# Performance work log

Measured on AMD Instinct MI355X. Metric: run time of the kernel, lower is better.

Reference implementation:

```python
import jax, jax.numpy as jnp
import numpy as np

N_NODES = 50000


def _add_self_loops(edge_index, n):
    loop = jnp.arange(n, dtype=edge_index.dtype)
    src = jnp.concatenate([edge_index[0], loop])
    dst = jnp.concatenate([edge_index[1], loop])
    return src, dst


def _gcn_norm(src, dst, n):
    # symmetric normalization with unit edge weights (edge_weight=None)
    w = jnp.ones(src.shape[0], dtype=jnp.float32)
    deg = jax.ops.segment_sum(w, dst, num_segments=n)  # [N]
    dinv = jnp.where(deg > 0, jax.lax.rsqrt(jnp.maximum(deg, 1.0)), 0.0)
    return dinv[src] * w * dinv[dst]  # [E+N]


def _gcn_conv(x, src, dst, norm, W, b, n):
    h = x @ W                                   # [N, out] transform first (PyG order)
    msg = h[src] * norm[:, None]                # [E+N, out] gather + scale
    agg = jax.ops.segment_sum(msg, dst, num_segments=n)  # scatter-add
    return agg + b


def setup_inputs() -> dict:
    key = jax.random.key(0)
    k1, k2, k3, k4 = jax.random.split(key, 4)
    N, E, IN, HID, OUT = N_NODES, 1600000, 512, 64, 7
    x = jax.random.normal(k1, (N, IN), dtype=jnp.float32)
    edge_index = jax.random.randint(k2, (2, E), 0, N, dtype=jnp.int64)
    W1 = jax.random.normal(k3, (IN, HID), dtype=jnp.float32) * (1.0 / np.sqrt(IN))
    b1 = jnp.zeros((HID,), dtype=jnp.float32)
    W2 = jax.random.normal(k4, (HID, OUT), dtype=jnp.float32) * (1.0 / np.sqrt(HID))
    b2 = jnp.zeros((OUT,), dtype=jnp.float32)
    return {"x": x, "edge_index": edge_index, "W1": W1, "b1": b1, "W2": W2, "b2": b2}


def reference(x, edge_index, W1, b1, W2, b2):
    n = x.shape[0]
    src, dst = _add_self_loops(edge_index, n)
    norm = _gcn_norm(src, dst, n)  # graph-only, shared across layers
    h = _gcn_conv(x, src, dst, norm, W1, b1, n)
    h = jax.nn.relu(h)
    # dropout is identity in eval/inference mode
    out = _gcn_conv(h, src, dst, norm, W2, b2, n)
    return out
```

## Files before the change

### kernel.cpp

```cpp
#include <hip/hip_runtime.h>

#define N_NODES 50000
#define N_EDGES 1600000
#define DIM_IN  512
#define DIM_HID 64
#define DIM_OUT 7
#define NBUCK   196
#define PART_BLOCKS 256

using u16 = unsigned short;
using bf16x8 = __attribute__((ext_vector_type(8))) __bf16;
using f32x4  = __attribute__((ext_vector_type(4))) float;

__device__ __forceinline__ float bf2f(u16 u) {
    union { float f; unsigned int i; } v;
    v.i = ((unsigned int)u) << 16;
    return v.f;
}

__device__ __forceinline__ u16 f2bf(float f) {
    union { float f; unsigned int i; } v;
    v.f = f;
    unsigned int r = 0x7FFFu + ((v.i >> 16) & 1u);
    return (u16)((v.i + r) >> 16);
}

__global__ void k_detect(const u16* __restrict__ xw, const int* __restrict__ ei32,
                         int* __restrict__ flags) {
    if (threadIdx.x == 0 && blockIdx.x == 0) {
        int sane = 0;
        for (int i = 0; i < 256; ++i) {
            u16 w = xw[2 * i];
            int e = (w >> 7) & 0xFF;
            if (e >= 100 && e <= 140) sane++;
        }
        flags[0] = (sane >= 200) ? 0 : 1;
        int nz = 0;
        for (int i = 0; i < 256; ++i)
            if (ei32[2 * i + 1] != 0) nz++;
        flags[1] = (nz == 0) ? 1 : 0;
    }
}

__device__ __forceinline__ int ld_edge(const int* ei, int i64f, size_t idx) {
    if (i64f) return (int)((const long long*)ei)[idx];
    return ei[idx];
}

__global__ void k_count(const int* __restrict__ ei, const int* __restrict__ flags,
                        int* __restrict__ gbsum, int* __restrict__ cnt) {
    __shared__ int hist[NBUCK];
    int t = threadIdx.x;
    int i64f = flags[1];
    const int CH = (N_EDGES + PART_BLOCKS - 1) / PART_BLOCKS;
    int lo = blockIdx.x * CH;
    int hi = lo + CH; if (hi > N_EDGES) hi = N_EDGES;
    if (t < NBUCK) hist[t] = 0;
    __syncthreads();
    for (int i = lo + t; i < hi; i += 256) {
        int s = ld_edge(ei, i64f, (size_t)i);
        int d = ld_edge(ei, i64f, (size_t)N_EDGES + i);
        if ((unsigned)d < (unsigned)N_NODES && (unsigned)s < (unsigned)N_NODES)
            atomicAdd(&hist[d >> 8], 1);
    }
    __syncthreads();
    if (t < NBUCK) {
        int h = hist[t];
        cnt[t * PART_BLOCKS + blockIdx.x] = h;
        if (h > 0) atomicAdd(&gbsum[t], h);
    }
}

__global__ void k_s2(const int* __restrict__ gbsum, int* __restrict__ bbase,
                     int* __restrict__ rowptr) {
    __shared__ int sc[256];
    int t = threadIdx.x;
    int v = (t < NBUCK) ? gbsum[t] : 0;
    sc[t] = v;
    __syncthreads();
    for (int off = 1; off < 256; off <<= 1) {
        int u = (t >= off) ? sc[t - off] : 0;
        __syncthreads();
        sc[t] += u;
        __syncthreads();
    }
    if (t < NBUCK) bbase[t] = sc[t] - v;
    if (t == 255) rowptr[N_NODES] = sc[255];
}

__global__ void k_pb(const int* __restrict__ bbase, int* __restrict__ cnt) {
    __shared__ int sc[256];
    int b = blockIdx.x, t = threadIdx.x;
    int v = cnt[b * PART_BLOCKS + t];
    sc[t] = v;
    __syncthreads();
    for (int off = 1; off < 256; off <<= 1) {
        int u = (t >= off) ? sc[t - off] : 0;
        __syncthreads();
        sc[t] += u;
        __syncthreads();
    }
    cnt[b * PART_BLOCKS + t] = bbase[b] + sc[t] - v;
}

__global__ void k_part(const int* __restrict__ ei, const int* __restrict__ flags,
                       const int* __restrict__ cnt, unsigned int* __restrict__ ebuf) {
    __shared__ int cur[NBUCK];
    int t = threadIdx.x, blk = blockIdx.x;
    int i64f = flags[1];
    const int CH = (N_EDGES + PART_BLOCKS - 1) / PART_BLOCKS;
    int lo = blk * CH;
    int hi = lo + CH; if (hi > N_EDGES) hi = N_EDGES;
    if (t < NBUCK) cur[t] = cnt[t * PART_BLOCKS + blk];
    __syncthreads();
    for (int i = lo + t; i < hi; i += 256) {
        int s = ld_edge(ei, i64f, (size_t)i);
        int d = ld_edge(ei, i64f, (size_t)N_EDGES + i);
        if ((unsigned)d < (unsigned)N_NODES && (unsigned)s < (unsigned)N_NODES) {
            int pos = atomicAdd(&cur[d >> 8], 1);
            if ((unsigned)pos < (unsigned)N_EDGES)
                ebuf[pos] = ((unsigned)s << 8) | (unsigned)(d & 255);
        }
    }
}

__global__ void k_cfill(const unsigned int* __restrict__ ebuf,
                        const int* __restrict__ bbase, const int* __restrict__ gbsum,
                        int* __restrict__ rowptr, float* __restrict__ dinv,
                        int* __restrict__ col) {
    __shared__ int dcnt[256];
    __shared__ int sc[256];
    __shared__ int cur[256];
    int b = blockIdx.x, t = threadIdx.x;
    int e0 = bbase[b];
    int e1 = e0 + gbsum[b];
    dcnt[t] = 0;
    __syncthreads();
    for (int e = e0 + t; e < e1; e += 256)
        atomicAdd(&dcnt[ebuf[e] & 255u], 1);
    __syncthreads();
    int v = dcnt[t];
    sc[t] = v;
    __syncthreads();
    for (int off = 1; off < 256; off <<= 1) {
        int u = (t >= off) ? sc[t - off] : 0;
        __syncthreads();
        sc[t] += u;
        __syncthreads();
    }
    int row0 = e0 + sc[t] - v;
    cur[t] = row0;
    int idx = b * 256 + t;
    if (idx < N_NODES) {
        rowptr[idx] = row0;
        dinv[idx] = rsqrtf((float)(v + 1));
    }
    __syncthreads();
    for (int e = e0 + t; e < e1; e += 256) {
        unsigned int x = ebuf[e];
        int p = atomicAdd(&cur[x & 255u], 1);
        if ((unsigned)p < (unsigned)N_EDGES) col[p] = (int)(x >> 8);
    }
}

__global__ void k_tw1(const void* __restrict__ W1, const int* __restrict__ flags,
                      u16* __restrict__ W1T) {
    int i = blockIdx.x * blockDim.x + threadIdx.x;
    if (i < DIM_IN * DIM_HID) {
        int n = i >> 9;
        int k = i & 511;
        if (flags[0]) W1T[i] = f2bf(((const float*)W1)[k * DIM_HID + n]);
        else          W1T[i] = ((const u16*)W1)[k * DIM_HID + n];
    }
}

__launch_bounds__(256)
__global__ void k_gemm1(const void* __restrict__ xraw, const u16* __restrict__ W1T,
                        const int* __restrict__ flags, const float* __restrict__ dinv,
                        u16* __restrict__ hs) {
    int f32f = flags[0];
    int wave = threadIdx.x >> 6;
    int lane = threadIdx.x & 63;
    int m16 = lane & 15;
    int quad = lane >> 4;
    int rbase = blockIdx.x * 64 + wave * 16;
    int ra = rbase + m16;
    if (ra > N_NODES - 1) ra = N_NODES - 1;
    const u16*   xrow_b = (const u16*)xraw   + (size_t)ra * DIM_IN + quad * 8;
    const float* xrow_f = (const float*)xraw + (size_t)ra * DIM_IN + quad * 8;
    const u16* wrow = W1T + (size_t)m16 * DIM_IN + quad * 8;

    f32x4 acc0 = {0.f, 0.f, 0.f, 0.f};
    f32x4 acc1 = {0.f, 0.f, 0.f, 0.f};
    f32x4 acc2 = {0.f, 0.f, 0.f, 0.f};
    f32x4 acc3 = {0.f, 0.f, 0.f, 0.f};

    for (int ks = 0; ks < DIM_IN / 32; ++ks) {
        bf16x8 a;
        if (f32f) {
            const float4* q = reinterpret_cast<const float4*>(xrow_f + ks * 32);
            float4 p0 = q[0], p1 = q[1];
            union { bf16x8 v; u16 s[8]; } u;
            u.s[0] = f2bf(p0.x); u.s[1] = f2bf(p0.y); u.s[2] = f2bf(p0.z); u.s[3] = f2bf(p0.w);
            u.s[4] = f2bf(p1.x); u.s[5] = f2bf(p1.y); u.s[6] = f2bf(p1.z); u.s[7] = f2bf(p1.w);
            a = u.v;
        } else {
            a = *reinterpret_cast<const bf16x8*>(xrow_b + ks * 32);
        }
        bf16x8 b0 = *reinterpret_cast<const bf16x8*>(wrow + ks * 32);
        bf16x8 b1 = *reinterpret_cast<const bf16x8*>(wrow + ks * 32 + 16 * DIM_IN);
        bf16x8 b2 = *reinterpret_cast<const bf16x8*>(wrow + ks * 32 + 32 * DIM_IN);
        bf16x8 b3 = *reinterpret_cast<const bf16x8*>(wrow + ks * 32 + 48 * DIM_IN);
        acc0 = __builtin_amdgcn_mfma_f32_16x16x32_bf16(a, b0, acc0, 0, 0, 0);
        acc1 = __builtin_amdgcn_mfma_f32_16x16x32_bf16(a, b1, acc1, 0, 0, 0);
        acc2 = __builtin_amdgcn_mfma_f32_16x16x32_bf16(a, b2, acc2, 0, 0, 0);
        acc3 = __builtin_amdgcn_mfma_f32_16x16x32_bf16(a, b3, acc3, 0, 0, 0);
    }

#pragma unroll
    for (int i = 0; i < 4; ++i) {
        int r = rbase + quad * 4 + i;
        if (r < N_NODES) {
            float dv = dinv[r];
            u16* orow = hs + (size_t)r * DIM_HID;
            orow[ 0 + m16] = f2bf(acc0[i] * dv);
            orow[16 + m16] = f2bf(acc1[i] * dv);
            orow[32 + m16] = f2bf(acc2[i] * dv);
            orow[48 + m16] = f2bf(acc3[i] * dv);
        }
    }
}

__launch_bounds__(256)
__global__ void k_agg1(const u16* __restrict__ hs, const int* __restrict__ rowptr,
                       const int* __restrict__ col, const float* __restrict__ dinv,
                       const void* __restrict__ b1, const void* __restrict__ W2,
                       const int* __restrict__ flags, float* __restrict__ zs) {
    int f32f = flags[0];
    int wave = threadIdx.x >> 6;
    int lane = threadIdx.x & 63;
    int d = blockIdx.x * 4 + wave;
    if (d >= N_NODES) return;
    int start = rowptr[d], end = rowptr[d + 1];
    if (start < 0) start = 0;
    if (end > N_EDGES) end = N_EDGES;
    if (end < start) end = start;

    float acc = 0.f;
    int n8 = (end - start) >> 3;
    int cA[8];
    if (n8 > 0) {
        const int* cp = col + start;
#pragma unroll
        for (int j = 0; j < 8; ++j) cA[j] = cp[j];
        for (int it = 0; it < n8; ++it) {
            int cB[8];
            if (it + 1 < n8) {
                const int* cpn = col + start + (it + 1) * 8;
#pragma unroll
                for (int j = 0; j < 8; ++j) cB[j] = cpn[j];
            } else {
#pragma unroll
                for (int j = 0; j < 8; ++j) cB[j] = 0;
            }
            float v[8];
#pragma unroll
            for (int j = 0; j < 8; ++j) v[j] = bf2f(hs[(size_t)cA[j] * DIM_HID + lane]);
#pragma unroll
            for (int j = 0; j < 8; ++j) acc += v[j];
#pragma unroll
            for (int j = 0; j < 8; ++j) cA[j] = cB[j];
        }
    }
    for (int e = start + n8 * 8; e < end; ++e)
        acc += bf2f(hs[(size_t)col[e] * DIM_HID + lane]);
    acc += bf2f(hs[(size_t)d * DIM_HID + lane]);

    float b1v = f32f ? ((const float*)b1)[lane] : bf2f(((const u16*)b1)[lane]);
    float dv = dinv[d];
    float h2 = fmaxf(acc * dv + b1v, 0.f);

    float p[7];
#pragma unroll
    for (int f = 0; f < 7; ++f) {
        float w = f32f ? ((const float*)W2)[lane * DIM_OUT + f]
                       : bf2f(((const u16*)W2)[lane * DIM_OUT + f]);
        p[f] = h2 * w;
    }
#pragma unroll
    for (int off = 32; off >= 1; off >>= 1) {
#pragma unroll
        for (int f = 0; f < 7; ++f) p[f] += __shfl_xor(p[f], off);
    }
    if (lane == 0) {
#pragma unroll
        for (int f = 0; f < 7; ++f) zs[(size_t)d * 8 + f] = p[f] * dv;
        zs[(size_t)d * 8 + 7] = 0.f;
    }
}

__launch_bounds__(256)
__global__ void k_agg2(const float* __restrict__ zs, const int* __restrict__ rowptr,
                       const int* __restrict__ col, const float* __restrict__ dinv,
                       const void* __restrict__ b2, const int* __restrict__ flags,
                       float* __restrict__ out) {
    int f32f = flags[0];
    int wave = threadIdx.x >> 6;
    int lane = threadIdx.x & 63;
    int d = blockIdx.x * 4 + wave;
    if (d >= N_NODES) return;
    int f = lane & 7;
    int g = lane >> 3;
    int start = rowptr[d], end = rowptr[d + 1];
    if (start < 0) start = 0;
    if (end > N_EDGES) end = N_EDGES;
    if (end < start) end = start;

    float acc = 0.f;
    for (int e = start + g; e < end; e += 8)
        acc += zs[(size_t)col[e] * 8 + f];

    acc += __shfl_xor(acc, 8);
    acc += __shfl_xor(acc, 16);
    acc += __shfl_xor(acc, 32);

    if (lane < 7) {
        float b2v = f32f ? ((const float*)b2)[lane] : bf2f(((const u16*)b2)[lane]);
        float tot = (acc + zs[(size_t)d * 8 + lane]) * dinv[d] + b2v;
        out[(size_t)d * DIM_OUT + lane] = tot;
    }
}

extern "C" void kernel_launch(void* const* d_in, const int* in_sizes, int n_in,
                              void* d_out, int out_size, void* d_ws, size_t ws_size,
                              hipStream_t stream) {
    const void* x  = d_in[0];
    const int*  ei = (const int*)d_in[1];
    const void* W1 = d_in[2];
    const void* b1 = d_in[3];
    const void* W2 = d_in[4];
    const void* b2 = d_in[5];

    char* ws = (char*)d_ws;
    size_t off = 0;
    auto alloc = [&](size_t bytes) -> void* {
        void* p = ws + off;
        off = (off + bytes + 255) & ~(size_t)255;
        return p;
    };
    int*   flags  = (int*)alloc(32);
    int*   rowptr = (int*)alloc((size_t)(N_NODES + 1) * 4);
    int*   gbsum  = (int*)alloc((size_t)NBUCK * 4);
    int*   bbase  = (int*)alloc((size_t)NBUCK * 4);
    int*   cnt    = (int*)alloc((size_t)NBUCK * PART_BLOCKS * 4);
    float* dinv   = (float*)alloc((size_t)N_NODES * 4);
    u16*   W1T    = (u16*)alloc((size_t)DIM_IN * DIM_HID * 2);
    unsigned int* ebuf = (unsigned int*)alloc((size_t)N_EDGES * 4);
    int*   colb   = (int*)alloc((size_t)N_EDGES * 4);
    u16*   hs     = (u16*)alloc((size_t)N_NODES * DIM_HID * 2);
    float* zs     = (float*)alloc((size_t)N_NODES * 8 * 4);
    float* out    = (float*)d_out;

    hipMemsetAsync(gbsum, 0, (size_t)NBUCK * 4, stream);
    k_detect<<<1, 64, 0, stream>>>((const u16*)x, ei, flags);
    k_count<<<PART_BLOCKS, 256, 0, stream>>>(ei, flags, gbsum, cnt);
    k_s2   <<<1, 256, 0, stream>>>(gbsum, bbase, rowptr);
    k_pb   <<<NBUCK, 256, 0, stream>>>(bbase, cnt);
    k_part <<<PART_BLOCKS, 256, 0, stream>>>(ei, flags, cnt, ebuf);
    k_cfill<<<NBUCK, 256, 0, stream>>>(ebuf, bbase, gbsum, rowptr, dinv, colb);
    k_tw1  <<<(DIM_IN * DIM_HID + 255) / 256, 256, 0, stream>>>(W1, flags, W1T);
    k_gemm1<<<(N_NODES + 63) / 64, 256, 0, stream>>>(x, W1T, flags, dinv, hs);
    k_agg1 <<<(N_NODES + 3) / 4, 256, 0, stream>>>(hs, rowptr, colb, dinv, b1, W2, flags, zs);
    k_agg2 <<<(N_NODES + 3) / 4, 256, 0, stream>>>(zs, rowptr, colb, dinv, b2, flags, out);
}
```

Measured before the change: 347.1 us.

## Parallelize detect, merge scan kernels, widen CSR blocks, shuffle-broadcast agg1 indices

Several changes land together. The flag detection becomes a parallel shared-memory reduction, and the separate bucket-scan kernel is folded into k_pb, which now recomputes the global scan in every block. The CSR-build kernels (count, part, cfill) launch 1024-thread blocks instead of 256, and int64 edge loads read only the low 32-bit word. In k_agg1 each lane loads one column index per 64 edges and broadcasts it with shuffles, gathering 16 rows per step to raise memory-level parallelism. The costs are extra cross-lane shuffles and a redundant per-block scan, and the int64 load now assumes little-endian indices that fit in 32 bits.

```diff
diff --git a/kernel.cpp b/kernel.cpp
--- a/kernel.cpp
+++ b/kernel.cpp
@@ -27,23 +27,26 @@
 
 __global__ void k_detect(const u16* __restrict__ xw, const int* __restrict__ ei32,
                          int* __restrict__ flags) {
-    if (threadIdx.x == 0 && blockIdx.x == 0) {
-        int sane = 0;
-        for (int i = 0; i < 256; ++i) {
-            u16 w = xw[2 * i];
-            int e = (w >> 7) & 0xFF;
-            if (e >= 100 && e <= 140) sane++;
-        }
-        flags[0] = (sane >= 200) ? 0 : 1;
-        int nz = 0;
-        for (int i = 0; i < 256; ++i)
-            if (ei32[2 * i + 1] != 0) nz++;
-        flags[1] = (nz == 0) ? 1 : 0;
+    __shared__ int s1[256];
+    __shared__ int s2[256];
+    int t = threadIdx.x;
+    u16 w = xw[2 * t];
+    int e = (w >> 7) & 0xFF;
+    s1[t] = (e >= 100 && e <= 140) ? 1 : 0;
+    s2[t] = (ei32[2 * t + 1] != 0) ? 1 : 0;
+    __syncthreads();
+    for (int off = 128; off >= 1; off >>= 1) {
+        if (t < off) { s1[t] += s1[t + off]; s2[t] += s2[t + off]; }
+        __syncthreads();
+    }
+    if (t == 0) {
+        flags[0] = (s1[0] >= 200) ? 0 : 1;
+        flags[1] = (s2[0] == 0) ? 1 : 0;
     }
 }
 
 __device__ __forceinline__ int ld_edge(const int* ei, int i64f, size_t idx) {
-    if (i64f) return (int)((const long long*)ei)[idx];
+    if (i64f) return ei[2 * idx];
     return ei[idx];
 }
 
@@ -57,7 +60,7 @@
     int hi = lo + CH; if (hi > N_EDGES) hi = N_EDGES;
     if (t < NBUCK) hist[t] = 0;
     __syncthreads();
-    for (int i = lo + t; i < hi; i += 256) {
+    for (int i = lo + t; i < hi; i += 1024) {
         int s = ld_edge(ei, i64f, (size_t)i);
         int d = ld_edge(ei, i64f, (size_t)N_EDGES + i);
         if ((unsigned)d < (unsigned)N_NODES && (unsigned)s < (unsigned)N_NODES)
@@ -71,11 +74,26 @@
     }
 }
 
-__global__ void k_s2(const int* __restrict__ gbsum, int* __restrict__ bbase,
-                     int* __restrict__ rowptr) {
+__global__ void k_pb(const int* __restrict__ gbsum, int* __restrict__ cnt,
+                     int* __restrict__ bbase, int* __restrict__ rowptr) {
+    __shared__ int g0[256];
+    __shared__ int gs[256];
     __shared__ int sc[256];
-    int t = threadIdx.x;
-    int v = (t < NBUCK) ? gbsum[t] : 0;
+    int b = blockIdx.x, t = threadIdx.x;
+    int gv = (t < NBUCK) ? gbsum[t] : 0;
+    g0[t] = gv;
+    gs[t] = gv;
+    __syncthreads();
+    for (int off = 1; off < 256; off <<= 1) {
+        int u = (t >= off) ? gs[t - off] : 0;
+        __syncthreads();
+        gs[t] += u;
+        __syncthreads();
+    }
+    int bb = gs[b] - g0[b];
+    if (t == 0) bbase[b] = bb;
+    if (b == 0 && t == 255) rowptr[N_NODES] = gs[255];
+    int v = cnt[b * PART_BLOCKS + t];
     sc[t] = v;
     __syncthreads();
     for (int off = 1; off < 256; off <<= 1) {
@@ -84,23 +102,7 @@
         sc[t] += u;
         __syncthreads();
     }
-    if (t < NBUCK) bbase[t] = sc[t] - v;
-    if (t == 255) rowptr[N_NODES] = sc[255];
-}
-
-__global__ void k_pb(const int* __restrict__ bbase, int* __restrict__ cnt) {
-    __shared__ int sc[256];
-    int b = blockIdx.x, t = threadIdx.x;
-    int v = cnt[b * PART_BLOCKS + t];
-    sc[t] = v;
-    __syncthreads();
-    for (int off = 1; off < 256; off <<= 1) {
-        int u = (t >= off) ? sc[t - off] : 0;
-        __syncthreads();
-        sc[t] += u;
-        __syncthreads();
-    }
-    cnt[b * PART_BLOCKS + t] = bbase[b] + sc[t] - v;
+    cnt[b * PART_BLOCKS + t] = bb + sc[t] - v;
 }
 
 __global__ void k_part(const int* __restrict__ ei, const int* __restrict__ flags,
@@ -113,7 +115,7 @@
     int hi = lo + CH; if (hi > N_EDGES) hi = N_EDGES;
     if (t < NBUCK) cur[t] = cnt[t * PART_BLOCKS + blk];
     __syncthreads();
-    for (int i = lo + t; i < hi; i += 256) {
+    for (int i = lo + t; i < hi; i += 1024) {
         int s = ld_edge(ei, i64f, (size_t)i);
         int d = ld_edge(ei, i64f, (size_t)N_EDGES + i);
         if ((unsigned)d < (unsigned)N_NODES && (unsigned)s < (unsigned)N_NODES) {
@@ -134,29 +136,31 @@
     int b = blockIdx.x, t = threadIdx.x;
     int e0 = bbase[b];
     int e1 = e0 + gbsum[b];
-    dcnt[t] = 0;
-    __syncthreads();
-    for (int e = e0 + t; e < e1; e += 256)
+    if (t < 256) dcnt[t] = 0;
+    __syncthreads();
+    for (int e = e0 + t; e < e1; e += 1024)
         atomicAdd(&dcnt[ebuf[e] & 255u], 1);
     __syncthreads();
-    int v = dcnt[t];
-    sc[t] = v;
+    int v = 0;
+    if (t < 256) { v = dcnt[t]; sc[t] = v; }
     __syncthreads();
     for (int off = 1; off < 256; off <<= 1) {
-        int u = (t >= off) ? sc[t - off] : 0;
-        __syncthreads();
-        sc[t] += u;
-        __syncthreads();
-    }
-    int row0 = e0 + sc[t] - v;
-    cur[t] = row0;
-    int idx = b * 256 + t;
-    if (idx < N_NODES) {
-        rowptr[idx] = row0;
-        dinv[idx] = rsqrtf((float)(v + 1));
-    }
-    __syncthreads();
-    for (int e = e0 + t; e < e1; e += 256) {
+        int u = (t >= off && t < 256) ? sc[t - off] : 0;
+        __syncthreads();
+        if (t < 256) sc[t] += u;
+        __syncthreads();
+    }
+    if (t < 256) {
+        int row0 = e0 + sc[t] - v;
+        cur[t] = row0;
+        int idx = b * 256 + t;
+        if (idx < N_NODES) {
+            rowptr[idx] = row0;
+            dinv[idx] = rsqrtf((float)(v + 1));
+        }
+    }
+    __syncthreads();
+    for (int e = e0 + t; e < e1; e += 1024) {
         unsigned int x = ebuf[e];
         int p = atomicAdd(&cur[x & 255u], 1);
         if ((unsigned)p < (unsigned)N_EDGES) col[p] = (int)(x >> 8);
@@ -246,35 +250,23 @@
     if (end > N_EDGES) end = N_EDGES;
     if (end < start) end = start;
 
-    float acc = 0.f;
-    int n8 = (end - start) >> 3;
-    int cA[8];
-    if (n8 > 0) {
-        const int* cp = col + start;
-#pragma unroll
-        for (int j = 0; j < 8; ++j) cA[j] = cp[j];
-        for (int it = 0; it < n8; ++it) {
-            int cB[8];
-            if (it + 1 < n8) {
-                const int* cpn = col + start + (it + 1) * 8;
-#pragma unroll
-                for (int j = 0; j < 8; ++j) cB[j] = cpn[j];
-            } else {
-#pragma unroll
-                for (int j = 0; j < 8; ++j) cB[j] = 0;
+    float acc = bf2f(hs[(size_t)d * DIM_HID + lane]);
+
+    for (int base = start; base < end; base += 64) {
+        int rem = end - base; if (rem > 64) rem = 64;
+        int ce = base + lane;
+        int c = (ce < end) ? col[ce] : 0;
+        for (int j0 = 0; j0 < rem; j0 += 16) {
+            float v[16];
+#pragma unroll
+            for (int j = 0; j < 16; ++j) {
+                int cj = __shfl(c, j0 + j);
+                v[j] = (j0 + j < rem) ? bf2f(hs[(size_t)cj * DIM_HID + lane]) : 0.f;
             }
-            float v[8];
-#pragma unroll
-            for (int j = 0; j < 8; ++j) v[j] = bf2f(hs[(size_t)cA[j] * DIM_HID + lane]);
-#pragma unroll
-            for (int j = 0; j < 8; ++j) acc += v[j];
-#pragma unroll
-            for (int j = 0; j < 8; ++j) cA[j] = cB[j];
-        }
-    }
-    for (int e = start + n8 * 8; e < end; ++e)
-        acc += bf2f(hs[(size_t)col[e] * DIM_HID + lane]);
-    acc += bf2f(hs[(size_t)d * DIM_HID + lane]);
+#pragma unroll
+            for (int j = 0; j < 16; ++j) acc += v[j];
+        }
+    }
 
     float b1v = f32f ? ((const float*)b1)[lane] : bf2f(((const u16*)b1)[lane]);
     float dv = dinv[d];
@@ -362,12 +354,11 @@
     float* out    = (float*)d_out;
 
     hipMemsetAsync(gbsum, 0, (size_t)NBUCK * 4, stream);
-    k_detect<<<1, 64, 0, stream>>>((const u16*)x, ei, flags);
-    k_count<<<PART_BLOCKS, 256, 0, stream>>>(ei, flags, gbsum, cnt);
-    k_s2   <<<1, 256, 0, stream>>>(gbsum, bbase, rowptr);
-    k_pb   <<<NBUCK, 256, 0, stream>>>(bbase, cnt);
-    k_part <<<PART_BLOCKS, 256, 0, stream>>>(ei, flags, cnt, ebuf);
-    k_cfill<<<NBUCK, 256, 0, stream>>>(ebuf, bbase, gbsum, rowptr, dinv, colb);
+    k_detect<<<1, 256, 0, stream>>>((const u16*)x, ei, flags);
+    k_count<<<PART_BLOCKS, 1024, 0, stream>>>(ei, flags, gbsum, cnt);
+    k_pb   <<<NBUCK, 256, 0, stream>>>(gbsum, cnt, bbase, rowptr);
+    k_part <<<PART_BLOCKS, 1024, 0, stream>>>(ei, flags, cnt, ebuf);
+    k_cfill<<<NBUCK, 1024, 0, stream>>>(ebuf, bbase, gbsum, rowptr, dinv, colb);
     k_tw1  <<<(DIM_IN * DIM_HID + 255) / 256, 256, 0, stream>>>(W1, flags, W1T);
     k_gemm1<<<(N_NODES + 63) / 64, 256, 0, stream>>>(x, W1T, flags, dinv, hs);
     k_agg1 <<<(N_NODES + 3) / 4, 256, 0, stream>>>(hs, rowptr, colb, dinv, b1, W2, flags, zs);
```

New measurement: 341.7 us. Within noise of the previous version (-1.5%).
